# Optimization experiments

Measured on AMD Instinct MI355X. Metric: run time of the kernel, lower is better.

The kernel has to match this reference:

```python
import jax, jax.numpy as jnp
import numpy as np
from jax import lax

EMBED_DIM = 384
NUM_GROUPS = 128
GROUP_SIZE = 64
LN_EPS = 1e-5


def setup_inputs() -> dict:
    key = jax.random.key(0)
    k_pts, k1, k2, k3, k4 = jax.random.split(key, 5)
    B, N = 32, 16384
    points = jax.random.normal(k_pts, (B, N, 3), dtype=jnp.float32)
    # local_mlp: Linear(3,128) -> GELU -> Linear(128, embed_dim)
    w1 = jax.random.normal(k1, (3, 128), dtype=jnp.float32) * (1.0 / np.sqrt(3))
    b1 = jax.random.normal(k2, (128,), dtype=jnp.float32) * 0.01
    w2 = jax.random.normal(k3, (128, EMBED_DIM), dtype=jnp.float32) * (1.0 / np.sqrt(128))
    b2 = jax.random.normal(k4, (EMBED_DIM,), dtype=jnp.float32) * 0.01
    ln_scale = jnp.ones((EMBED_DIM,), dtype=jnp.float32)
    ln_bias = jnp.zeros((EMBED_DIM,), dtype=jnp.float32)
    return {"points": points, "w1": w1, "b1": b1, "w2": w2, "b2": b2,
            "ln_scale": ln_scale, "ln_bias": ln_bias}


def _farthest_point_sample(points, num_samples):
    # points: [B, N, 3]. Deterministic start at index 0 (torch uses randint).
    B, N, _ = points.shape

    def step(carry, _):
        distance, farthest = carry  # [B, N], [B]
        centroid = jnp.take_along_axis(points, farthest[:, None, None], axis=1)  # [B,1,3]
        d = jnp.sum((points - centroid) ** 2, axis=-1)  # [B, N]
        distance = jnp.minimum(distance, d)
        nxt = jnp.argmax(distance, axis=-1).astype(jnp.int32)
        return (distance, nxt), farthest

    init = (jnp.full((B, N), jnp.inf, dtype=points.dtype),
            jnp.zeros((B,), dtype=jnp.int32))
    _, idx = lax.scan(step, init, None, length=num_samples)  # [S, B]
    return idx.T  # [B, S]


def reference(points, w1, b1, w2, b2, ln_scale, ln_bias):
    B, N, _ = points.shape
    centroid_idx = _farthest_point_sample(points, NUM_GROUPS)  # [B, G]
    centroids = jnp.take_along_axis(
        points, centroid_idx[:, :, None].astype(jnp.int32), axis=1)  # [B, G, 3]

    # squared distances (same ordering as torch.cdist for topk); matmul form
    # avoids materializing a [B, G, N, 3] diff tensor.
    c2 = jnp.sum(centroids ** 2, axis=-1)  # [B, G]
    p2 = jnp.sum(points ** 2, axis=-1)     # [B, N]
    dist2 = c2[:, :, None] + p2[:, None, :] - 2.0 * jnp.einsum(
        'bgc,bnc->bgn', centroids, points)  # [B, G, N]

    # k smallest -> top_k of negated distances
    _, neighbor_idx = lax.top_k(-dist2, GROUP_SIZE)  # [B, G, K]

    batch_ix = jnp.arange(B)[:, None, None]
    grouped = points[batch_ix, neighbor_idx]  # [B, G, K, 3]
    local_coords = grouped - centroids[:, :, None, :]  # [B, G, K, 3]

    h = jax.nn.gelu(local_coords @ w1 + b1, approximate=False)  # [B,G,K,128]
    feats = h @ w2 + b2  # [B, G, K, D]
    tokens = jnp.mean(feats, axis=2)  # [B, G, D]

    mu = jnp.mean(tokens, axis=-1, keepdims=True)
    var = jnp.mean((tokens - mu) ** 2, axis=-1, keepdims=True)
    tokens_ln = (tokens - mu) * lax.rsqrt(var + LN_EPS) * ln_scale + ln_bias
    return centroids, tokens_ln
```

## Files before the change

### kernel.cpp

```cpp
#include <hip/hip_runtime.h>
#include <math.h>

#define BB 32
#define NN 16384
#define GG 128
#define KK 64
#define HH 128
#define DD 384
#define LN_EPS 1e-5f
#define NBUCK 2048
#define CANDCAP 1024

__device__ __forceinline__ float sq3(float x, float y, float z) {
    return __fadd_rn(__fadd_rn(__fmul_rn(x, x), __fmul_rn(y, y)), __fmul_rn(z, z));
}

__device__ __forceinline__ unsigned distkey(float px, float py, float pz, float4 c4) {
    float p2 = sq3(px, py, pz);
    float dot = __fadd_rn(__fadd_rn(__fmul_rn(c4.x, px), __fmul_rn(c4.y, py)),
                          __fmul_rn(c4.z, pz));
    float d = __fsub_rn(__fadd_rn(c4.w, p2), __fmul_rn(2.0f, dot));
    unsigned u = __float_as_uint(d);
    return u ^ ((u & 0x80000000u) ? 0xFFFFFFFFu : 0x80000000u);
}

__global__ void prep_kernel(const float* __restrict__ w2, float* __restrict__ w2t) {
    int i = blockIdx.x * 256 + threadIdx.x;
    if (i < HH * DD) {
        int f = i >> 7;
        int k = i & 127;
        w2t[i] = w2[k * DD + f];
    }
}

__global__ __launch_bounds__(512) void fps_kernel(const float* __restrict__ pts,
                                                  float* __restrict__ cent_out,
                                                  float4* __restrict__ cent_pad) {
    __shared__ float4 xl[NN / 4];
    __shared__ float4 yl[NN / 4];
    __shared__ unsigned long long slot[GG];

    const int b = blockIdx.x;
    const int tid = threadIdx.x;
    const float* p = pts + (size_t)b * NN * 3;
    const float4* p4 = (const float4*)p;

    float z[32], dist[32];
#pragma unroll
    for (int j = 0; j < 8; j++) {
        int q = j * 512 + tid;
        float4 A = p4[3 * q], B = p4[3 * q + 1], C = p4[3 * q + 2];
        xl[q] = make_float4(A.x, A.w, B.z, C.y);
        yl[q] = make_float4(A.y, B.x, B.w, C.z);
        z[j * 4 + 0] = A.z; z[j * 4 + 1] = B.y; z[j * 4 + 2] = C.x; z[j * 4 + 3] = C.w;
#pragma unroll
        for (int t = 0; t < 4; t++) dist[j * 4 + t] = INFINITY;
    }
    for (int i = tid; i < GG; i += 512) slot[i] = 0ull;
    __syncthreads();

    float cx = p[0], cy = p[1], cz = p[2];

    for (int it = 0; it < GG; it++) {
        if (tid == 0) {
            float* co = cent_out + ((size_t)b * GG + it) * 3;
            co[0] = cx; co[1] = cy; co[2] = cz;
            cent_pad[b * GG + it] = make_float4(cx, cy, cz, sq3(cx, cy, cz));
        }
        if (it == GG - 1) break;

        float bv0 = -INFINITY, bv1 = -INFINITY, bv2 = -INFINITY, bv3 = -INFINITY;
        int bi0 = 0, bi1 = 0, bi2 = 0, bi3 = 0;
#pragma unroll
        for (int j = 0; j < 8; j++) {
            int q = j * 512 + tid;
            int nb = 4 * q;
            float4 xs = xl[q];
            float4 ys = yl[q];
            {
                float dx = __fsub_rn(xs.x, cx);
                float dy = __fsub_rn(ys.x, cy);
                float dz = __fsub_rn(z[j * 4 + 0], cz);
                float d = sq3(dx, dy, dz);
                float dj = fminf(dist[j * 4 + 0], d);
                dist[j * 4 + 0] = dj;
                if (dj > bv0) { bv0 = dj; bi0 = nb + 0; }
            }
            {
                float dx = __fsub_rn(xs.y, cx);
                float dy = __fsub_rn(ys.y, cy);
                float dz = __fsub_rn(z[j * 4 + 1], cz);
                float d = sq3(dx, dy, dz);
                float dj = fminf(dist[j * 4 + 1], d);
                dist[j * 4 + 1] = dj;
                if (dj > bv1) { bv1 = dj; bi1 = nb + 1; }
            }
            {
                float dx = __fsub_rn(xs.z, cx);
                float dy = __fsub_rn(ys.z, cy);
                float dz = __fsub_rn(z[j * 4 + 2], cz);
                float d = sq3(dx, dy, dz);
                float dj = fminf(dist[j * 4 + 2], d);
                dist[j * 4 + 2] = dj;
                if (dj > bv2) { bv2 = dj; bi2 = nb + 2; }
            }
            {
                float dx = __fsub_rn(xs.w, cx);
                float dy = __fsub_rn(ys.w, cy);
                float dz = __fsub_rn(z[j * 4 + 3], cz);
                float d = sq3(dx, dy, dz);
                float dj = fminf(dist[j * 4 + 3], d);
                dist[j * 4 + 3] = dj;
                if (dj > bv3) { bv3 = dj; bi3 = nb + 3; }
            }
        }
        float fv = bv0; int fi = bi0;
        if (bv1 > fv || (bv1 == fv && bi1 < fi)) { fv = bv1; fi = bi1; }
        if (bv2 > fv || (bv2 == fv && bi2 < fi)) { fv = bv2; fi = bi2; }
        if (bv3 > fv || (bv3 == fv && bi3 < fi)) { fv = bv3; fi = bi3; }
#pragma unroll
        for (int off = 32; off >= 1; off >>= 1) {
            float ov = __shfl_down(fv, off);
            int oi = __shfl_down(fi, off);
            if (ov > fv || (ov == fv && oi < fi)) { fv = ov; fi = oi; }
        }
        if ((tid & 63) == 0) {
            unsigned long long packed =
                ((unsigned long long)__float_as_uint(fv) << 32) |
                (unsigned)(0xFFFFFFFFu - (unsigned)fi);
            atomicMax(&slot[it], packed);
        }
        __syncthreads();
        unsigned long long w = slot[it];
        int idx = (int)(0xFFFFFFFFu - (unsigned)w);
        const float* wp = p + (size_t)idx * 3;
        cx = wp[0]; cy = wp[1]; cz = wp[2];
    }
}

__global__ __launch_bounds__(256, 6) void group_kernel(
    const float* __restrict__ pts, const float4* __restrict__ cent_pad,
    const float* __restrict__ w1, const float* __restrict__ b1,
    const float* __restrict__ w2t, const float* __restrict__ b2,
    const float* __restrict__ lns, const float* __restrict__ lnb,
    float* __restrict__ tok_out) {
    __shared__ __align__(16) union {
        unsigned hist[NBUCK];
        unsigned long long cand[CANDCAP];
    } sh;
    __shared__ int selIdx[KK];
    __shared__ float4 localPt[KK];
    __shared__ float w1s[3 * HH];
    __shared__ float b1s[HH];
    __shared__ __align__(16) float hbar[HH];
    __shared__ float partial[256];
    __shared__ float red2[8];
    __shared__ float toks[DD];
    __shared__ int waveSum[4];
    __shared__ unsigned long long wmin[4];
    __shared__ unsigned TA_S;
    __shared__ int cntS;
    __shared__ unsigned long long lastS;
    __shared__ float muS, rstdS;

    const int tid = threadIdx.x;
    int bid = blockIdx.x;
    int xcd = bid & 7, sub = bid >> 3;
    int b = xcd * 4 + (sub >> 7);
    int g = sub & 127;

    const float* p = pts + (size_t)b * NN * 3;
    const float4* p4 = (const float4*)p;
    float4 c4 = cent_pad[b * GG + g];

    for (int i = tid; i < 3 * HH; i += 256) w1s[i] = w1[i];
    if (tid < HH) b1s[tid] = b1[tid];
    for (int i = tid; i < NBUCK; i += 256) sh.hist[i] = 0;
    if (tid == 0) cntS = 0;
    __syncthreads();

    for (int i = 0; i < 16; i++) {
        int t4 = i * 256 + tid;
        float4 A = p4[3 * t4], B = p4[3 * t4 + 1], C = p4[3 * t4 + 2];
        unsigned k0 = distkey(A.x, A.y, A.z, c4);
        unsigned k1 = distkey(A.w, B.x, B.y, c4);
        unsigned k2 = distkey(B.z, B.w, C.x, c4);
        unsigned k3 = distkey(C.y, C.z, C.w, c4);
        atomicAdd(&sh.hist[k0 >> 21], 1u);
        atomicAdd(&sh.hist[k1 >> 21], 1u);
        atomicAdd(&sh.hist[k2 >> 21], 1u);
        atomicAdd(&sh.hist[k3 >> 21], 1u);
    }
    __syncthreads();

    {
        uint4 h0 = ((const uint4*)sh.hist)[tid * 2];
        uint4 h1 = ((const uint4*)sh.hist)[tid * 2 + 1];
        int loc[8] = {(int)h0.x, (int)h0.y, (int)h0.z, (int)h0.w,
                      (int)h1.x, (int)h1.y, (int)h1.z, (int)h1.w};
        int s = 0;
#pragma unroll
        for (int j = 0; j < 8; j++) s += loc[j];
        int lane = tid & 63, wid = tid >> 6;
        int v = s;
#pragma unroll
        for (int off = 1; off < 64; off <<= 1) {
            int o = __shfl_up(v, off);
            if (lane >= off) v += o;
        }
        if (lane == 63) waveSum[wid] = v;
        __syncthreads();
        int base = 0;
        for (int w = 0; w < wid; w++) base += waveSum[w];
        int c = base + v - s;
#pragma unroll
        for (int j = 0; j < 8; j++) {
            if (c < KK && c + loc[j] >= KK) TA_S = (unsigned)(tid * 8 + j);
            c += loc[j];
        }
        __syncthreads();
    }
    unsigned TA = TA_S;

    for (int i = 0; i < 16; i++) {
        int t4 = i * 256 + tid;
        float4 A = p4[3 * t4], B = p4[3 * t4 + 1], C = p4[3 * t4 + 2];
        unsigned k[4];
        k[0] = distkey(A.x, A.y, A.z, c4);
        k[1] = distkey(A.w, B.x, B.y, c4);
        k[2] = distkey(B.z, B.w, C.x, c4);
        k[3] = distkey(C.y, C.z, C.w, c4);
#pragma unroll
        for (int q = 0; q < 4; q++) {
            if ((k[q] >> 21) <= TA) {
                int pos = atomicAdd(&cntS, 1);
                if (pos < CANDCAP)
                    sh.cand[pos] =
                        ((unsigned long long)k[q] << 32) | (unsigned)(4 * t4 + q);
            }
        }
    }
    __syncthreads();
    int cnt = cntS;

    if (cnt <= CANDCAP) {
        for (int c0 = tid; c0 < cnt; c0 += 256) {
            unsigned long long pr = sh.cand[c0];
            int rank = 0;
            for (int j = 0; j < cnt; j++) rank += (sh.cand[j] < pr);
            if (rank < KK) selIdx[rank] = (int)(unsigned)pr;
        }
        __syncthreads();
    } else {
        if (tid == 0) lastS = 0ull;
        __syncthreads();
        for (int r = 0; r < KK; r++) {
            unsigned long long last = lastS;
            unsigned long long best = 0xFFFFFFFFFFFFFFFFull;
            for (int i = 0; i < 16; i++) {
                int t4 = i * 256 + tid;
                float4 A = p4[3 * t4], B = p4[3 * t4 + 1], C = p4[3 * t4 + 2];
                unsigned k[4];
                k[0] = distkey(A.x, A.y, A.z, c4);
                k[1] = distkey(A.w, B.x, B.y, c4);
                k[2] = distkey(B.z, B.w, C.x, c4);
                k[3] = distkey(C.y, C.z, C.w, c4);
#pragma unroll
                for (int q = 0; q < 4; q++) {
                    unsigned long long pr =
                        ((unsigned long long)k[q] << 32) | (unsigned)(4 * t4 + q);
                    if ((r == 0 || pr > last) && pr < best) best = pr;
                }
            }
            unsigned blo = (unsigned)best, bhi = (unsigned)(best >> 32);
#pragma unroll
            for (int off = 32; off >= 1; off >>= 1) {
                unsigned olo = __shfl_down(blo, off);
                unsigned ohi = __shfl_down(bhi, off);
                unsigned long long ob = ((unsigned long long)ohi << 32) | olo;
                unsigned long long cur = ((unsigned long long)bhi << 32) | blo;
                if (ob < cur) { blo = olo; bhi = ohi; }
            }
            int lane = tid & 63, wid = tid >> 6;
            if (lane == 0) wmin[wid] = ((unsigned long long)bhi << 32) | blo;
            __syncthreads();
            if (tid == 0) {
                unsigned long long m = wmin[0];
                for (int w = 1; w < 4; w++) if (wmin[w] < m) m = wmin[w];
                selIdx[r] = (int)(unsigned)m;
                lastS = m;
            }
            __syncthreads();
        }
    }

    if (tid < KK) {
        int n = selIdx[tid];
        float px = p[n * 3], py = p[n * 3 + 1], pz = p[n * 3 + 2];
        localPt[tid] = make_float4(px - c4.x, py - c4.y, pz - c4.z, 0.f);
    }
    __syncthreads();
    {
        int f = tid & 127, half = tid >> 7;
        float wa = w1s[f], wb = w1s[HH + f], wc = w1s[2 * HH + f], bb = b1s[f];
        float s = 0.f;
        for (int k = half * 32; k < half * 32 + 32; k++) {
            float4 lp = localPt[k];
            float a = lp.x * wa + lp.y * wb + lp.z * wc + bb;
            float hh = 0.5f * a * (1.0f + erff(a * 0.70710678118654752440f));
            s += hh;
        }
        partial[tid] = s;
    }
    __syncthreads();
    if (tid < HH) hbar[tid] = (partial[tid] + partial[tid + HH]) * (1.0f / 64.0f);
    __syncthreads();
    for (int f2 = tid; f2 < DD; f2 += 256) {
        const float4* wrow = (const float4*)(w2t + f2 * HH);
        const float4* hb = (const float4*)hbar;
        float acc = b2[f2];
#pragma unroll 8
        for (int q = 0; q < 32; q++) {
            float4 w4 = wrow[q];
            float4 h4 = hb[q];
            acc += h4.x * w4.x + h4.y * w4.y + h4.z * w4.z + h4.w * w4.w;
        }
        toks[f2] = acc;
    }
    __syncthreads();
    {
        float s1 = 0.f, s2 = 0.f;
        for (int f2 = tid; f2 < DD; f2 += 256) {
            float v = toks[f2];
            s1 += v;
            s2 += v * v;
        }
#pragma unroll
        for (int off = 32; off >= 1; off >>= 1) {
            s1 += __shfl_down(s1, off);
            s2 += __shfl_down(s2, off);
        }
        int lane = tid & 63, wid = tid >> 6;
        if (lane == 0) { partial[wid] = s1; red2[wid] = s2; }
        __syncthreads();
        if (tid == 0) {
            float t1 = partial[0] + partial[1] + partial[2] + partial[3];
            float t2 = red2[0] + red2[1] + red2[2] + red2[3];
            float mu = t1 / (float)DD;
            float var = t2 / (float)DD - mu * mu;
            muS = mu;
            rstdS = rsqrtf(var + LN_EPS);
        }
        __syncthreads();
    }
    float mu = muS, rstd = rstdS;
    float* outp = tok_out + ((size_t)b * GG + g) * DD;
    for (int f2 = tid; f2 < DD; f2 += 256) {
        outp[f2] = (toks[f2] - mu) * rstd * lns[f2] + lnb[f2];
    }
}

extern "C" void kernel_launch(void* const* d_in, const int* in_sizes, int n_in,
                              void* d_out, int out_size, void* d_ws, size_t ws_size,
                              hipStream_t stream) {
    const float* pts = (const float*)d_in[0];
    const float* w1 = (const float*)d_in[1];
    const float* b1 = (const float*)d_in[2];
    const float* w2 = (const float*)d_in[3];
    const float* b2 = (const float*)d_in[4];
    const float* lns = (const float*)d_in[5];
    const float* lnb = (const float*)d_in[6];
    float* out = (float*)d_out;

    float4* cent_pad = (float4*)d_ws;
    float* w2t = (float*)((char*)d_ws + BB * GG * sizeof(float4));

    prep_kernel<<<192, 256, 0, stream>>>(w2, w2t);
    fps_kernel<<<BB, 512, 0, stream>>>(pts, out, cent_pad);
    group_kernel<<<BB * GG, 256, 0, stream>>>(pts, cent_pad, w1, b1, w2t, b2, lns, lnb,
                                              out + BB * GG * 3);
}
```

Before: 541.8 us.

## Widen FPS to 1024 threads and replace atomic argmax with per-wave double-buffered keys

The farthest-point-sampling kernel now runs 1024 threads per batch, so each thread holds half as many points in registers. The per-iteration block argmax drops the shared atomicMax. Each wave writes its packed key to a double-buffered shared slot, and every thread scans the 16 slots after one barrier, which removes the second sync hazard. The next centroid's coordinates come from shared x/y arrays and a wave-supplied z value instead of a global memory load. The risk is that the serial 16-entry scan in every thread, plus the larger block, offsets the shorter per-thread loop.

```diff
diff --git a/kernel.cpp b/kernel.cpp
--- a/kernel.cpp
+++ b/kernel.cpp
@@ -33,22 +33,23 @@
     }
 }
 
-__global__ __launch_bounds__(512) void fps_kernel(const float* __restrict__ pts,
-                                                  float* __restrict__ cent_out,
-                                                  float4* __restrict__ cent_pad) {
+__global__ __launch_bounds__(1024) void fps_kernel(const float* __restrict__ pts,
+                                                   float* __restrict__ cent_out,
+                                                   float4* __restrict__ cent_pad) {
     __shared__ float4 xl[NN / 4];
     __shared__ float4 yl[NN / 4];
-    __shared__ unsigned long long slot[GG];
+    __shared__ unsigned long long wkey[2][16];
+    __shared__ float wzs[2][16];
 
     const int b = blockIdx.x;
     const int tid = threadIdx.x;
     const float* p = pts + (size_t)b * NN * 3;
     const float4* p4 = (const float4*)p;
 
-    float z[32], dist[32];
-#pragma unroll
-    for (int j = 0; j < 8; j++) {
-        int q = j * 512 + tid;
+    float z[16], dist[16];
+#pragma unroll
+    for (int j = 0; j < 4; j++) {
+        int q = j * 1024 + tid;
         float4 A = p4[3 * q], B = p4[3 * q + 1], C = p4[3 * q + 2];
         xl[q] = make_float4(A.x, A.w, B.z, C.y);
         yl[q] = make_float4(A.y, B.x, B.w, C.z);
@@ -56,10 +57,10 @@
 #pragma unroll
         for (int t = 0; t < 4; t++) dist[j * 4 + t] = INFINITY;
     }
-    for (int i = tid; i < GG; i += 512) slot[i] = 0ull;
     __syncthreads();
 
     float cx = p[0], cy = p[1], cz = p[2];
+    const int wid = tid >> 6;
 
     for (int it = 0; it < GG; it++) {
         if (tid == 0) {
@@ -68,12 +69,13 @@
             cent_pad[b * GG + it] = make_float4(cx, cy, cz, sq3(cx, cy, cz));
         }
         if (it == GG - 1) break;
+        const int par = it & 1;
 
         float bv0 = -INFINITY, bv1 = -INFINITY, bv2 = -INFINITY, bv3 = -INFINITY;
         int bi0 = 0, bi1 = 0, bi2 = 0, bi3 = 0;
 #pragma unroll
-        for (int j = 0; j < 8; j++) {
-            int q = j * 512 + tid;
+        for (int j = 0; j < 4; j++) {
+            int q = j * 1024 + tid;
             int nb = 4 * q;
             float4 xs = xl[q];
             float4 ys = yl[q];
@@ -114,27 +116,48 @@
                 if (dj > bv3) { bv3 = dj; bi3 = nb + 3; }
             }
         }
-        float fv = bv0; int fi = bi0;
-        if (bv1 > fv || (bv1 == fv && bi1 < fi)) { fv = bv1; fi = bi1; }
-        if (bv2 > fv || (bv2 == fv && bi2 < fi)) { fv = bv2; fi = bi2; }
-        if (bv3 > fv || (bv3 == fv && bi3 < fi)) { fv = bv3; fi = bi3; }
+        float mfv = bv0; int mfi = bi0;
+        if (bv1 > mfv || (bv1 == mfv && bi1 < mfi)) { mfv = bv1; mfi = bi1; }
+        if (bv2 > mfv || (bv2 == mfv && bi2 < mfi)) { mfv = bv2; mfi = bi2; }
+        if (bv3 > mfv || (bv3 == mfv && bi3 < mfi)) { mfv = bv3; mfi = bi3; }
+
+        float fv = mfv; int fi = mfi;
 #pragma unroll
         for (int off = 32; off >= 1; off >>= 1) {
             float ov = __shfl_down(fv, off);
             int oi = __shfl_down(fi, off);
             if (ov > fv || (ov == fv && oi < fi)) { fv = ov; fi = oi; }
         }
-        if ((tid & 63) == 0) {
-            unsigned long long packed =
-                ((unsigned long long)__float_as_uint(fv) << 32) |
-                (unsigned)(0xFFFFFFFFu - (unsigned)fi);
-            atomicMax(&slot[it], packed);
-        }
-        __syncthreads();
-        unsigned long long w = slot[it];
-        int idx = (int)(0xFFFFFFFFu - (unsigned)w);
-        const float* wp = p + (size_t)idx * 3;
-        cx = wp[0]; cy = wp[1]; cz = wp[2];
+        int wfi = __shfl(fi, 0);
+        if (mfi == wfi) {
+            int jj = (wfi >> 2) - tid;
+            int tt = wfi & 3;
+            float sz = 0.f;
+#pragma unroll
+            for (int j = 0; j < 4; j++) {
+                if (jj == j * 1024) {
+#pragma unroll
+                    for (int t = 0; t < 4; t++) {
+                        if (tt == t) sz = z[j * 4 + t];
+                    }
+                }
+            }
+            wkey[par][wid] = ((unsigned long long)__float_as_uint(mfv) << 32) |
+                             (unsigned)(0xFFFFFFFFu - (unsigned)mfi);
+            wzs[par][wid] = sz;
+        }
+        __syncthreads();
+        unsigned long long bk = wkey[par][0];
+        int bw = 0;
+#pragma unroll
+        for (int w = 1; w < 16; w++) {
+            unsigned long long k2 = wkey[par][w];
+            if (k2 > bk) { bk = k2; bw = w; }
+        }
+        int idx = (int)(0xFFFFFFFFu - (unsigned)bk);
+        cx = ((const float*)xl)[idx];
+        cy = ((const float*)yl)[idx];
+        cz = wzs[par][bw];
     }
 }
 
@@ -376,7 +399,7 @@
     float* w2t = (float*)((char*)d_ws + BB * GG * sizeof(float4));
 
     prep_kernel<<<192, 256, 0, stream>>>(w2, w2t);
-    fps_kernel<<<BB, 512, 0, stream>>>(pts, out, cent_pad);
+    fps_kernel<<<BB, 1024, 0, stream>>>(pts, out, cent_pad);
     group_kernel<<<BB * GG, 256, 0, stream>>>(pts, cent_pad, w1, b1, w2t, b2, lns, lnb,
                                               out + BB * GG * 3);
 }
```

New measurement: 636.8 us. 17.5% more time.
